# Optimization experiments

Hardware: AMD Instinct MI355X
Metric: run time of the kernel (lower is better)

The kernel has to match this reference:

```python
import jax, jax.numpy as jnp
import numpy as np

N_QUBITS = 4
N_LAYERS = 6
NUM_CLASSES = 10


def _apply_1q(state, gate, wire):
    # state: (B,2,2,2,2); gate: (2,2) shared or (B,2,2) per-sample
    s = jnp.moveaxis(state, wire + 1, -1)
    if gate.ndim == 3:
        s = jnp.einsum('bij,b...j->b...i', gate, s)
    else:
        s = jnp.einsum('ij,b...j->b...i', gate, s)
    return jnp.moveaxis(s, -1, wire + 1)


def _apply_cnot(state, c, t):
    s = jnp.moveaxis(state, (c + 1, t + 1), (-2, -1))
    s = jnp.stack([s[..., 0, :], s[..., 1, ::-1]], axis=-2)
    return jnp.moveaxis(s, (-2, -1), (c + 1, t + 1))


def _rot(phi, theta, omega):
    # PennyLane Rot = RZ(omega) @ RY(theta) @ RZ(phi)
    c, s = jnp.cos(theta / 2), jnp.sin(theta / 2)
    ep = jnp.exp(-0.5j * (phi + omega))
    em = jnp.exp(-0.5j * (phi - omega))
    return jnp.stack([
        jnp.stack([ep * c, -jnp.conj(em) * s]),
        jnp.stack([em * s, jnp.conj(ep) * c]),
    ])


def _quantum_net(angles, q_weights):
    # batched default.qubit statevector simulation, 4 wires
    B = angles.shape[0]
    state = jnp.zeros((B, 2, 2, 2, 2), jnp.complex64).at[:, 0, 0, 0, 0].set(1.0)
    # AngleEmbedding, rotation='Y' (per-sample RY gates)
    for w in range(N_QUBITS):
        a = angles[:, w]
        c, s = jnp.cos(a / 2), jnp.sin(a / 2)
        g = jnp.stack([jnp.stack([c, -s], -1), jnp.stack([s, c], -1)], -2)
        state = _apply_1q(state, g.astype(jnp.complex64), w)
    # StronglyEntanglingLayers: Rot on each wire, then ring of CNOTs with range r
    for l in range(N_LAYERS):
        for w in range(N_QUBITS):
            state = _apply_1q(state, _rot(q_weights[l, w, 0], q_weights[l, w, 1], q_weights[l, w, 2]), w)
        r = l % (N_QUBITS - 1) + 1
        for w in range(N_QUBITS):
            state = _apply_cnot(state, w, (w + r) % N_QUBITS)
    probs = jnp.abs(state) ** 2  # (B,2,2,2,2)
    z = jnp.array([1.0, -1.0], dtype=probs.dtype)
    exps = [jnp.einsum('bijkl,' + 'ijkl'[w] + '->b', probs, z) for w in range(N_QUBITS)]
    return jnp.stack(exps, -1)  # (B,4) expval PauliZ per wire


def setup_inputs() -> dict:
    key = jax.random.key(0)
    ks = jax.random.split(key, 6)
    B = 65536
    x = jax.random.normal(ks[0], (B, 512), jnp.float32)
    W_pre = jax.random.normal(ks[1], (N_QUBITS, 512), jnp.float32) / np.sqrt(512)
    b_pre = jax.random.normal(ks[2], (N_QUBITS,), jnp.float32) * 0.01
    q_weights = 0.01 * jax.random.normal(ks[3], (N_LAYERS, N_QUBITS, 3), jnp.float32)
    W_post = jax.random.normal(ks[4], (NUM_CLASSES, N_QUBITS), jnp.float32) / np.sqrt(N_QUBITS)
    b_post = jax.random.normal(ks[5], (NUM_CLASSES,), jnp.float32) * 0.01
    return {'x': x, 'W_pre': W_pre, 'b_pre': b_pre, 'q_weights': q_weights,
            'W_post': W_post, 'b_post': b_post}


def reference(x, W_pre, b_pre, q_weights, W_post, b_post):
    pre = x @ W_pre.T + b_pre                 # (B,4)
    angles = jnp.tanh(pre) * np.float32(np.pi)
    q_out = _quantum_net(angles, q_weights)   # (B,4)
    return q_out @ W_post.T + b_post          # (B,10)
```

## Files before the change

### kernel.cpp

```cpp
#include <hip/hip_runtime.h>
#include <math.h>

#define K 512
#define K4 128
#define NQ 4
#define NL 6
#define NC 10

__device__ __forceinline__ float dpp_xor1(float v) {
    return __int_as_float(__builtin_amdgcn_mov_dpp(__float_as_int(v), 0xB1, 0xF, 0xF, true));
}
__device__ __forceinline__ float dpp_xor2(float v) {
    return __int_as_float(__builtin_amdgcn_mov_dpp(__float_as_int(v), 0x4E, 0xF, 0xF, true));
}

#define A_BLOCK 256
#define A_WAVES 4
#define A_ROWS_PER_WAVE 16
#define A_ROWS_PER_BLOCK 64
#define A_PAIRS 8
#define PART_STRIDE 68

__global__ __launch_bounds__(A_BLOCK, 4) void prenet_kernel(
    const float* __restrict__ x,
    const float* __restrict__ W_pre,
    const float* __restrict__ b_pre,
    float* __restrict__ angles)
{
    __shared__ float part[A_ROWS_PER_BLOCK * PART_STRIDE];

    const int tid  = threadIdx.x;
    const int wave = tid >> 6;
    const int lane = tid & 63;

    const float4* x4 = (const float4*)x;
    const float4* W4 = (const float4*)W_pre;
    const float4 w0a = W4[0 * K4 + lane], w0b = W4[0 * K4 + 64 + lane];
    const float4 w1a = W4[1 * K4 + lane], w1b = W4[1 * K4 + 64 + lane];
    const float4 w2a = W4[2 * K4 + lane], w2b = W4[2 * K4 + 64 + lane];
    const float4 w3a = W4[3 * K4 + lane], w3b = W4[3 * K4 + 64 + lane];

    const int rowBase = blockIdx.x * A_ROWS_PER_BLOCK + wave * A_ROWS_PER_WAVE;

    const int partOff = (lane & 3) * 16 + (lane >> 2);

    float4 bufa[2][2], bufb[2][2];
    {
        const float4* r0 = x4 + (size_t)(rowBase + 0) * K4;
        const float4* r1 = x4 + (size_t)(rowBase + 1) * K4;
        bufa[0][0] = r0[lane]; bufb[0][0] = r0[64 + lane];
        bufa[0][1] = r1[lane]; bufb[0][1] = r1[64 + lane];
    }

    #pragma unroll
    for (int p = 0; p < A_PAIRS; ++p) {
        const int cp = p & 1, np = cp ^ 1;
        if (p + 1 < A_PAIRS) {
            const float4* r0 = x4 + (size_t)(rowBase + 2 * p + 2) * K4;
            const float4* r1 = x4 + (size_t)(rowBase + 2 * p + 3) * K4;
            bufa[np][0] = r0[lane]; bufb[np][0] = r0[64 + lane];
            bufa[np][1] = r1[lane]; bufb[np][1] = r1[64 + lane];
        }
        #pragma unroll
        for (int rr = 0; rr < 2; ++rr) {
            const float4 xa = bufa[cp][rr];
            const float4 xb = bufb[cp][rr];
            float acc0 = xa.x * w0a.x + xa.y * w0a.y + xa.z * w0a.z + xa.w * w0a.w
                       + xb.x * w0b.x + xb.y * w0b.y + xb.z * w0b.z + xb.w * w0b.w;
            float acc1 = xa.x * w1a.x + xa.y * w1a.y + xa.z * w1a.z + xa.w * w1a.w
                       + xb.x * w1b.x + xb.y * w1b.y + xb.z * w1b.z + xb.w * w1b.w;
            float acc2 = xa.x * w2a.x + xa.y * w2a.y + xa.z * w2a.z + xa.w * w2a.w
                       + xb.x * w2b.x + xb.y * w2b.y + xb.z * w2b.z + xb.w * w2b.w;
            float acc3 = xa.x * w3a.x + xa.y * w3a.y + xa.z * w3a.z + xa.w * w3a.w
                       + xb.x * w3b.x + xb.y * w3b.y + xb.z * w3b.z + xb.w * w3b.w;

            const bool b0 = (lane & 1);
            float pA = b0 ? acc1 : acc0;
            float qA = b0 ? acc0 : acc1;
            pA += dpp_xor1(qA);
            float pB = b0 ? acc3 : acc2;
            float qB = b0 ? acc2 : acc3;
            pB += dpp_xor1(qB);
            const bool b1 = (lane & 2);
            float pv = b1 ? pB : pA;
            float qv = b1 ? pA : pB;
            pv += dpp_xor2(qv);

            part[(wave * A_ROWS_PER_WAVE + 2 * p + rr) * PART_STRIDE + partOff] = pv;
        }
    }
    __syncthreads();

    {
        const int row  = tid >> 2;
        const int wire = tid & 3;
        const float4* seg4 = (const float4*)&part[row * PART_STRIDE + wire * 16];
        const float4 s0 = seg4[0], s1 = seg4[1], s2 = seg4[2], s3 = seg4[3];
        const float s = ((s0.x + s0.y) + (s0.z + s0.w))
                      + ((s1.x + s1.y) + (s1.z + s1.w))
                      + ((s2.x + s2.y) + (s2.z + s2.w))
                      + ((s3.x + s3.y) + (s3.z + s3.w));
        const float z = s + b_pre[wire];
        const float e = __expf(2.f * z);
        const float th = 1.f - 2.f / (e + 1.f);
        angles[(size_t)blockIdx.x * A_ROWS_PER_BLOCK * NQ + tid] =
            th * 3.14159265358979323846f;
    }
}

#define B_BLOCK 256

__global__ __launch_bounds__(B_BLOCK, 4) void vqc_kernel(
    const float* __restrict__ angles,
    const float* __restrict__ q_weights,
    const float* __restrict__ W_post,
    const float* __restrict__ b_post,
    float* __restrict__ out)
{
    __shared__ float gates[NL * NQ][8];
    __shared__ float Wpost_s[NC * NQ];
    __shared__ float bpost_s[NC];

    const int tid = threadIdx.x;

    if (tid < NL * NQ) {
        const int l = tid >> 2, w = tid & 3;
        const float phi = q_weights[l * 12 + w * 3 + 0];
        const float th  = q_weights[l * 12 + w * 3 + 1];
        const float om  = q_weights[l * 12 + w * 3 + 2];
        const float c  = cosf(0.5f * th), s = sinf(0.5f * th);
        const float hp = 0.5f * (phi + om), hm = 0.5f * (phi - om);
        const float epr = cosf(hp), epi = -sinf(hp);
        const float emr = cosf(hm), emi = -sinf(hm);
        gates[tid][0] =  epr * c;  gates[tid][1] =  epi * c;
        gates[tid][2] = -emr * s;  gates[tid][3] =  emi * s;
        gates[tid][4] =  emr * s;  gates[tid][5] =  emi * s;
        gates[tid][6] =  epr * c;  gates[tid][7] = -epi * c;
    }
    if (tid >= 64 && tid < 64 + NC * NQ) Wpost_s[tid - 64] = W_post[tid - 64];
    if (tid >= 104 && tid < 104 + NC)    bpost_s[tid - 104] = b_post[tid - 104];
    __syncthreads();

    const int r = blockIdx.x * B_BLOCK + tid;
    const float4 a = ((const float4*)angles)[r];

    float c0, s0, c1, s1, c2, s2, c3, s3;
    __sincosf(0.5f * a.x, &s0, &c0);
    __sincosf(0.5f * a.y, &s1, &c1);
    __sincosf(0.5f * a.z, &s2, &c2);
    __sincosf(0.5f * a.w, &s3, &c3);

    float ar[16], ai[16];
    #pragma unroll
    for (int i = 0; i < 16; ++i) {
        ar[i] = ((i & 8) ? s0 : c0) * ((i & 4) ? s1 : c1)
              * ((i & 2) ? s2 : c2) * ((i & 1) ? s3 : c3);
        ai[i] = 0.f;
    }

    #pragma unroll
    for (int l = 0; l < NL; ++l) {
        #pragma unroll
        for (int w = 0; w < NQ; ++w) {
            const float* G = gates[l * 4 + w];
            const float g00r = G[0], g00i = G[1], g01r = G[2], g01i = G[3];
            const float g10r = G[4], g10i = G[5], g11r = G[6], g11i = G[7];
            const int m = 8 >> w;
            #pragma unroll
            for (int i0 = 0; i0 < 16; ++i0) {
                if (i0 & m) continue;
                const int i1 = i0 | m;
                const float A0r = ar[i0], A0i = ai[i0];
                const float A1r = ar[i1], A1i = ai[i1];
                ar[i0] = g00r * A0r - g00i * A0i + g01r * A1r - g01i * A1i;
                ai[i0] = g00r * A0i + g00i * A0r + g01r * A1i + g01i * A1r;
                ar[i1] = g10r * A0r - g10i * A0i + g11r * A1r - g11i * A1i;
                ai[i1] = g10r * A0i + g10i * A0r + g11r * A1i + g11i * A1r;
            }
        }
        const int rshift = l % 3 + 1;
        #pragma unroll
        for (int w = 0; w < NQ; ++w) {
            const int cm = 8 >> w;
            const int tm = 8 >> ((w + rshift) & 3);
            #pragma unroll
            for (int i = 0; i < 16; ++i) {
                if ((i & cm) && !(i & tm)) {
                    const int ii = i | tm;
                    float t;
                    t = ar[i]; ar[i] = ar[ii]; ar[ii] = t;
                    t = ai[i]; ai[i] = ai[ii]; ai[ii] = t;
                }
            }
        }
    }

    float e0 = 0.f, e1 = 0.f, e2 = 0.f, e3 = 0.f;
    #pragma unroll
    for (int i = 0; i < 16; ++i) {
        const float pr = ar[i] * ar[i] + ai[i] * ai[i];
        e0 += (i & 8) ? -pr : pr;
        e1 += (i & 4) ? -pr : pr;
        e2 += (i & 2) ? -pr : pr;
        e3 += (i & 1) ? -pr : pr;
    }

    float o[NC];
    #pragma unroll
    for (int c = 0; c < NC; ++c) {
        o[c] = bpost_s[c]
             + Wpost_s[c * 4 + 0] * e0 + Wpost_s[c * 4 + 1] * e1
             + Wpost_s[c * 4 + 2] * e2 + Wpost_s[c * 4 + 3] * e3;
    }
    float2* orow2 = (float2*)(out + (size_t)r * NC);
    #pragma unroll
    for (int c = 0; c < 5; ++c)
        orow2[c] = make_float2(o[2 * c], o[2 * c + 1]);
}

extern "C" void kernel_launch(void* const* d_in, const int* in_sizes, int n_in,
                              void* d_out, int out_size, void* d_ws, size_t ws_size,
                              hipStream_t stream) {
    const float* x         = (const float*)d_in[0];
    const float* W_pre     = (const float*)d_in[1];
    const float* b_pre     = (const float*)d_in[2];
    const float* q_weights = (const float*)d_in[3];
    const float* W_post    = (const float*)d_in[4];
    const float* b_post    = (const float*)d_in[5];
    float* out    = (float*)d_out;
    float* angles = (float*)d_ws;

    const int B = in_sizes[0] / K;
    dim3 gridA(B / A_ROWS_PER_BLOCK);
    prenet_kernel<<<gridA, A_BLOCK, 0, stream>>>(x, W_pre, b_pre, angles);
    dim3 gridB(B / B_BLOCK);
    vqc_kernel<<<gridB, B_BLOCK, 0, stream>>>(angles, q_weights, W_post, b_post, out);
}
```

Baseline: 208.0 us.

## Fuse pre-net projection and quantum simulation into a single kernel

Merges the projection/tanh kernel and the statevector simulation kernel into one launch. Angles now pass through shared memory instead of a global workspace, which removes one launch and the angle write and read. In the fused block, only the first 64 of 256 threads (one wave) run the simulation, so that compute is serialised per block and can add latency behind the memory-bound projection phase.

Result: no change. 209.2 us (+0.6%).

```diff
diff --git a/kernel.cpp b/kernel.cpp
--- a/kernel.cpp
+++ b/kernel.cpp
@@ -21,17 +21,39 @@
 #define A_PAIRS 8
 #define PART_STRIDE 68
 
-__global__ __launch_bounds__(A_BLOCK, 4) void prenet_kernel(
+__global__ __launch_bounds__(A_BLOCK, 4) void vqc_fused_kernel(
     const float* __restrict__ x,
     const float* __restrict__ W_pre,
     const float* __restrict__ b_pre,
-    float* __restrict__ angles)
+    const float* __restrict__ q_weights,
+    const float* __restrict__ W_post,
+    const float* __restrict__ b_post,
+    float* __restrict__ out)
 {
     __shared__ float part[A_ROWS_PER_BLOCK * PART_STRIDE];
+    __shared__ float angles_s[A_ROWS_PER_BLOCK][NQ];
+    __shared__ float4 gates4[NL * NQ][2];
+    __shared__ float Wpost_s[NC * NQ];
+    __shared__ float bpost_s[NC];
 
     const int tid  = threadIdx.x;
     const int wave = tid >> 6;
     const int lane = tid & 63;
+
+    if (tid < NL * NQ) {
+        const int l = tid >> 2, w = tid & 3;
+        const float phi = q_weights[l * 12 + w * 3 + 0];
+        const float th  = q_weights[l * 12 + w * 3 + 1];
+        const float om  = q_weights[l * 12 + w * 3 + 2];
+        const float c  = cosf(0.5f * th), s = sinf(0.5f * th);
+        const float hp = 0.5f * (phi + om), hm = 0.5f * (phi - om);
+        const float epr = cosf(hp), epi = -sinf(hp);
+        const float emr = cosf(hm), emi = -sinf(hm);
+        gates4[tid][0] = make_float4( epr * c,  epi * c, -emr * s,  emi * s);
+        gates4[tid][1] = make_float4( emr * s,  emi * s,  epr * c, -epi * c);
+    }
+    if (tid >= 64 && tid < 64 + NC * NQ) Wpost_s[tid - 64] = W_post[tid - 64];
+    if (tid >= 104 && tid < 104 + NC)    bpost_s[tid - 104] = b_post[tid - 104];
 
     const float4* x4 = (const float4*)x;
     const float4* W4 = (const float4*)W_pre;
@@ -41,7 +63,6 @@
     const float4 w3a = W4[3 * K4 + lane], w3b = W4[3 * K4 + 64 + lane];
 
     const int rowBase = blockIdx.x * A_ROWS_PER_BLOCK + wave * A_ROWS_PER_WAVE;
-
     const int partOff = (lane & 3) * 16 + (lane >> 2);
 
     float4 bufa[2][2], bufb[2][2];
@@ -103,119 +124,89 @@
         const float z = s + b_pre[wire];
         const float e = __expf(2.f * z);
         const float th = 1.f - 2.f / (e + 1.f);
-        angles[(size_t)blockIdx.x * A_ROWS_PER_BLOCK * NQ + tid] =
-            th * 3.14159265358979323846f;
-    }
-}
-
-#define B_BLOCK 256
-
-__global__ __launch_bounds__(B_BLOCK, 4) void vqc_kernel(
-    const float* __restrict__ angles,
-    const float* __restrict__ q_weights,
-    const float* __restrict__ W_post,
-    const float* __restrict__ b_post,
-    float* __restrict__ out)
-{
-    __shared__ float gates[NL * NQ][8];
-    __shared__ float Wpost_s[NC * NQ];
-    __shared__ float bpost_s[NC];
-
-    const int tid = threadIdx.x;
-
-    if (tid < NL * NQ) {
-        const int l = tid >> 2, w = tid & 3;
-        const float phi = q_weights[l * 12 + w * 3 + 0];
-        const float th  = q_weights[l * 12 + w * 3 + 1];
-        const float om  = q_weights[l * 12 + w * 3 + 2];
-        const float c  = cosf(0.5f * th), s = sinf(0.5f * th);
-        const float hp = 0.5f * (phi + om), hm = 0.5f * (phi - om);
-        const float epr = cosf(hp), epi = -sinf(hp);
-        const float emr = cosf(hm), emi = -sinf(hm);
-        gates[tid][0] =  epr * c;  gates[tid][1] =  epi * c;
-        gates[tid][2] = -emr * s;  gates[tid][3] =  emi * s;
-        gates[tid][4] =  emr * s;  gates[tid][5] =  emi * s;
-        gates[tid][6] =  epr * c;  gates[tid][7] = -epi * c;
-    }
-    if (tid >= 64 && tid < 64 + NC * NQ) Wpost_s[tid - 64] = W_post[tid - 64];
-    if (tid >= 104 && tid < 104 + NC)    bpost_s[tid - 104] = b_post[tid - 104];
+        angles_s[row][wire] = th * 3.14159265358979323846f;
+    }
     __syncthreads();
 
-    const int r = blockIdx.x * B_BLOCK + tid;
-    const float4 a = ((const float4*)angles)[r];
-
-    float c0, s0, c1, s1, c2, s2, c3, s3;
-    __sincosf(0.5f * a.x, &s0, &c0);
-    __sincosf(0.5f * a.y, &s1, &c1);
-    __sincosf(0.5f * a.z, &s2, &c2);
-    __sincosf(0.5f * a.w, &s3, &c3);
-
-    float ar[16], ai[16];
-    #pragma unroll
-    for (int i = 0; i < 16; ++i) {
-        ar[i] = ((i & 8) ? s0 : c0) * ((i & 4) ? s1 : c1)
-              * ((i & 2) ? s2 : c2) * ((i & 1) ? s3 : c3);
-        ai[i] = 0.f;
-    }
-
-    #pragma unroll
-    for (int l = 0; l < NL; ++l) {
-        #pragma unroll
-        for (int w = 0; w < NQ; ++w) {
-            const float* G = gates[l * 4 + w];
-            const float g00r = G[0], g00i = G[1], g01r = G[2], g01i = G[3];
-            const float g10r = G[4], g10i = G[5], g11r = G[6], g11i = G[7];
-            const int m = 8 >> w;
+    if (tid < A_ROWS_PER_BLOCK) {
+        const int rl = tid;
+        const int r  = blockIdx.x * A_ROWS_PER_BLOCK + rl;
+        const float a0 = angles_s[rl][0], a1 = angles_s[rl][1];
+        const float a2 = angles_s[rl][2], a3 = angles_s[rl][3];
+        float c0, s0, c1, s1, c2, s2, c3, s3;
+        __sincosf(0.5f * a0, &s0, &c0);
+        __sincosf(0.5f * a1, &s1, &c1);
+        __sincosf(0.5f * a2, &s2, &c2);
+        __sincosf(0.5f * a3, &s3, &c3);
+
+        float ar[16], ai[16];
+        #pragma unroll
+        for (int i = 0; i < 16; ++i) {
+            ar[i] = ((i & 8) ? s0 : c0) * ((i & 4) ? s1 : c1)
+                  * ((i & 2) ? s2 : c2) * ((i & 1) ? s3 : c3);
+            ai[i] = 0.f;
+        }
+
+        #pragma unroll
+        for (int l = 0; l < NL; ++l) {
             #pragma unroll
-            for (int i0 = 0; i0 < 16; ++i0) {
-                if (i0 & m) continue;
-                const int i1 = i0 | m;
-                const float A0r = ar[i0], A0i = ai[i0];
-                const float A1r = ar[i1], A1i = ai[i1];
-                ar[i0] = g00r * A0r - g00i * A0i + g01r * A1r - g01i * A1i;
-                ai[i0] = g00r * A0i + g00i * A0r + g01r * A1i + g01i * A1r;
-                ar[i1] = g10r * A0r - g10i * A0i + g11r * A1r - g11i * A1i;
-                ai[i1] = g10r * A0i + g10i * A0r + g11r * A1i + g11i * A1r;
-            }
-        }
-        const int rshift = l % 3 + 1;
-        #pragma unroll
-        for (int w = 0; w < NQ; ++w) {
-            const int cm = 8 >> w;
-            const int tm = 8 >> ((w + rshift) & 3);
-            #pragma unroll
-            for (int i = 0; i < 16; ++i) {
-                if ((i & cm) && !(i & tm)) {
-                    const int ii = i | tm;
-                    float t;
-                    t = ar[i]; ar[i] = ar[ii]; ar[ii] = t;
-                    t = ai[i]; ai[i] = ai[ii]; ai[ii] = t;
+            for (int w = 0; w < NQ; ++w) {
+                const float4 G0 = gates4[l * 4 + w][0];
+                const float4 G1 = gates4[l * 4 + w][1];
+                const float g00r = G0.x, g00i = G0.y, g01r = G0.z, g01i = G0.w;
+                const float g10r = G1.x, g10i = G1.y, g11r = G1.z, g11i = G1.w;
+                const int m = 8 >> w;
+                #pragma unroll
+                for (int i0 = 0; i0 < 16; ++i0) {
+                    if (i0 & m) continue;
+                    const int i1 = i0 | m;
+                    const float A0r = ar[i0], A0i = ai[i0];
+                    const float A1r = ar[i1], A1i = ai[i1];
+                    ar[i0] = g00r * A0r - g00i * A0i + g01r * A1r - g01i * A1i;
+                    ai[i0] = g00r * A0i + g00i * A0r + g01r * A1i + g01i * A1r;
+                    ar[i1] = g10r * A0r - g10i * A0i + g11r * A1r - g11i * A1i;
+                    ai[i1] = g10r * A0i + g10i * A0r + g11r * A1i + g11i * A1r;
                 }
             }
-        }
-    }
-
-    float e0 = 0.f, e1 = 0.f, e2 = 0.f, e3 = 0.f;
-    #pragma unroll
-    for (int i = 0; i < 16; ++i) {
-        const float pr = ar[i] * ar[i] + ai[i] * ai[i];
-        e0 += (i & 8) ? -pr : pr;
-        e1 += (i & 4) ? -pr : pr;
-        e2 += (i & 2) ? -pr : pr;
-        e3 += (i & 1) ? -pr : pr;
-    }
-
-    float o[NC];
-    #pragma unroll
-    for (int c = 0; c < NC; ++c) {
-        o[c] = bpost_s[c]
-             + Wpost_s[c * 4 + 0] * e0 + Wpost_s[c * 4 + 1] * e1
-             + Wpost_s[c * 4 + 2] * e2 + Wpost_s[c * 4 + 3] * e3;
-    }
-    float2* orow2 = (float2*)(out + (size_t)r * NC);
-    #pragma unroll
-    for (int c = 0; c < 5; ++c)
-        orow2[c] = make_float2(o[2 * c], o[2 * c + 1]);
+            const int rshift = l % 3 + 1;
+            #pragma unroll
+            for (int w = 0; w < NQ; ++w) {
+                const int cm = 8 >> w;
+                const int tm = 8 >> ((w + rshift) & 3);
+                #pragma unroll
+                for (int i = 0; i < 16; ++i) {
+                    if ((i & cm) && !(i & tm)) {
+                        const int ii = i | tm;
+                        float t;
+                        t = ar[i]; ar[i] = ar[ii]; ar[ii] = t;
+                        t = ai[i]; ai[i] = ai[ii]; ai[ii] = t;
+                    }
+                }
+            }
+        }
+
+        float e0 = 0.f, e1 = 0.f, e2 = 0.f, e3 = 0.f;
+        #pragma unroll
+        for (int i = 0; i < 16; ++i) {
+            const float pr = ar[i] * ar[i] + ai[i] * ai[i];
+            e0 += (i & 8) ? -pr : pr;
+            e1 += (i & 4) ? -pr : pr;
+            e2 += (i & 2) ? -pr : pr;
+            e3 += (i & 1) ? -pr : pr;
+        }
+
+        float o[NC];
+        #pragma unroll
+        for (int c = 0; c < NC; ++c) {
+            o[c] = bpost_s[c]
+                 + Wpost_s[c * 4 + 0] * e0 + Wpost_s[c * 4 + 1] * e1
+                 + Wpost_s[c * 4 + 2] * e2 + Wpost_s[c * 4 + 3] * e3;
+        }
+        float2* orow2 = (float2*)(out + (size_t)r * NC);
+        #pragma unroll
+        for (int c = 0; c < 5; ++c)
+            orow2[c] = make_float2(o[2 * c], o[2 * c + 1]);
+    }
 }
 
 extern "C" void kernel_launch(void* const* d_in, const int* in_sizes, int n_in,
@@ -227,12 +218,10 @@
     const float* q_weights = (const float*)d_in[3];
     const float* W_post    = (const float*)d_in[4];
     const float* b_post    = (const float*)d_in[5];
-    float* out    = (float*)d_out;
-    float* angles = (float*)d_ws;
+    float* out = (float*)d_out;
 
     const int B = in_sizes[0] / K;
-    dim3 gridA(B / A_ROWS_PER_BLOCK);
-    prenet_kernel<<<gridA, A_BLOCK, 0, stream>>>(x, W_pre, b_pre, angles);
-    dim3 gridB(B / B_BLOCK);
-    vqc_kernel<<<gridB, B_BLOCK, 0, stream>>>(angles, q_weights, W_post, b_post, out);
-}
+    dim3 grid(B / A_ROWS_PER_BLOCK);
+    vqc_fused_kernel<<<grid, A_BLOCK, 0, stream>>>(x, W_pre, b_pre, q_weights,
+                                                   W_post, b_post, out);
+}
```
